# Kernel optimization log

Measured on AMD Instinct MI355X. Metric: run time of the kernel, lower is better.

The kernel has to match this reference:

```python
import jax, jax.numpy as jnp
import numpy as np

B, N, C, G, K = 4, 6000, 91, 32, 100
IMG = 800.0
SCORE_TH = 0.05
NMS_TH = 0.5
MATCH_TH = 0.5
MIN_SIZE = 0.01
BBOX_CLIP = float(np.log(1000.0 / 16.0))
WX, WY, WW, WH = 10.0, 10.0, 5.0, 5.0


def _make_boxes(key, shape_prefix):
    k1, k2 = jax.random.split(key)
    xy = jax.random.uniform(k1, shape_prefix + (2,), minval=0.0, maxval=IMG - 130.0)
    wh = jax.random.uniform(k2, shape_prefix + (2,), minval=8.0, maxval=128.0)
    return jnp.concatenate([xy, xy + wh], axis=-1)


def setup_inputs() -> dict:
    key = jax.random.key(0)
    k1, k2, k3, k4, k5 = jax.random.split(key, 5)
    return {
        "class_logits": 2.0 * jax.random.normal(k1, (B * N, C), dtype=jnp.float32),
        "box_regression": jax.random.normal(k2, (B * N, C * 4), dtype=jnp.float32),
        "proposals": _make_boxes(k3, (B, N)),
        "gt_boxes": _make_boxes(k4, (B, G)),
        "gt_labels": jax.random.randint(k5, (B, G), 1, C),
    }


def _box_iou(a, b):
    # a [G,4], b [N,4] -> [G,N]
    area_a = (a[:, 2] - a[:, 0]) * (a[:, 3] - a[:, 1])
    area_b = (b[:, 2] - b[:, 0]) * (b[:, 3] - b[:, 1])
    lt = jnp.maximum(a[:, None, :2], b[None, :, :2])
    rb = jnp.minimum(a[:, None, 2:], b[None, :, 2:])
    wh = jnp.clip(rb - lt, 0.0)
    inter = wh[..., 0] * wh[..., 1]
    return inter / (area_a[:, None] + area_b[None, :] - inter)


def _decode(rel, props):
    # torchvision BoxCoder.decode; rel [N,C,4], props [N,4]
    w = props[:, 2] - props[:, 0]
    h = props[:, 3] - props[:, 1]
    cx = props[:, 0] + 0.5 * w
    cy = props[:, 1] + 0.5 * h
    dx = rel[..., 0] / WX
    dy = rel[..., 1] / WY
    dw = jnp.minimum(rel[..., 2] / WW, BBOX_CLIP)
    dh = jnp.minimum(rel[..., 3] / WH, BBOX_CLIP)
    pcx = dx * w[:, None] + cx[:, None]
    pcy = dy * h[:, None] + cy[:, None]
    pw = jnp.exp(dw) * w[:, None]
    ph = jnp.exp(dh) * h[:, None]
    return jnp.stack([pcx - 0.5 * pw, pcy - 0.5 * ph, pcx + 0.5 * pw, pcy + 0.5 * ph], axis=-1)


def _image(logits, reg, props, gtb, gtl):
    # --- assign_targets_to_proposals (Matcher, low=high=0.5, no low-quality matches) ---
    iou = _box_iou(gtb, props)                      # [G, N]
    best = iou.max(axis=0)
    mi = jnp.argmax(iou, axis=0)
    matched = jnp.where(best >= MATCH_TH, mi, -1)   # -1 == BELOW_LOW_THRESHOLD
    assigned = jnp.where(matched >= 0, gtl[jnp.clip(matched, 0)], 0)

    # --- postprocess_detections ---
    scores = jax.nn.softmax(logits, axis=-1)[:, 1:].reshape(-1)                       # [N*(C-1)]
    boxes = jnp.clip(_decode(reg.reshape(N, C, 4), props)[:, 1:], 0.0, IMG)
    boxes = boxes.reshape(-1, 4)                                                      # [N*(C-1),4]
    labels = jnp.tile(jnp.arange(1, C), N)                                            # [N*(C-1)]
    ws = boxes[:, 2] - boxes[:, 0]
    hs = boxes[:, 3] - boxes[:, 1]
    valid = (scores > SCORE_TH) & (ws >= MIN_SIZE) & (hs >= MIN_SIZE)
    s0 = jnp.where(valid, scores, -jnp.inf)
    # batched_nms trick: offset boxes by label so cross-class IoU is 0
    off = boxes + (labels.astype(boxes.dtype) * (IMG + 1.0))[:, None]
    off_area = (off[:, 2] - off[:, 0]) * (off[:, 3] - off[:, 1])

    def step(s, _):
        i = jnp.argmax(s)
        sc = s[i]
        b = off[i]
        lt = jnp.maximum(off[:, :2], b[:2])
        rb = jnp.minimum(off[:, 2:], b[2:])
        wh = jnp.clip(rb - lt, 0.0)
        inter = wh[:, 0] * wh[:, 1]
        iou_all = inter / (off_area + (b[2] - b[0]) * (b[3] - b[1]) - inter)
        s = jnp.where(iou_all > NMS_TH, -jnp.inf, s)  # suppress (includes self)
        ok = jnp.isfinite(sc)
        ob = jnp.where(ok, boxes[i], 0.0)
        osc = jnp.where(ok, sc, 0.0)
        ol = jnp.where(ok, labels[i], -1)
        return s, (ob, osc, ol)

    _, (kb, ksc, kl) = jax.lax.scan(step, s0, None, length=K)
    return kb, ksc, kl, assigned, matched


def reference(class_logits, box_regression, proposals, gt_boxes, gt_labels):
    logits = class_logits.reshape(B, N, C)
    reg = box_regression.reshape(B, N, C * 4)
    kb, ksc, kl, assigned, matched = jax.vmap(_image)(logits, reg, proposals, gt_boxes, gt_labels)
    dets = jnp.concatenate([kb, ksc[..., None]], axis=-1)  # [B, K, 5]
    return dets, kl, assigned, matched
```

## Files before the change

### kernel.cpp

```cpp
#include <hip/hip_runtime.h>
#include <math.h>

#define NB 4
#define NN 6000
#define NC 91
#define NG 32
#define NK 100
#define NCLS (NC - 1)
#define NBUC (NB * NCLS)
#define NWRD 94
#define NWRD_P 96
#define PMAX 512
#define MATW 256
#define MPB 4096
#define RS_BLOCKS 6000

#define SCORE_TH 0.05f
#define NMS_TH 0.5f
#define MATCH_TH 0.5f
#define MIN_SIZE 0.01f
#define BBOX_CLIP 4.135166556742356f
#define C_SUP 0.5000000298023223876953125

#define CFENCE() asm volatile("" ::: "memory")

__device__ __forceinline__ bool decode_one(
    const float* __restrict__ reg, const float* __restrict__ props,
    float l, float m, float s0, int row, int c, float out[5])
{
    float score = __fdiv_rn(expf(__fsub_rn(l, m)), s0);

    const float4 p = *reinterpret_cast<const float4*>(props + (size_t)row * 4);
    float w  = __fsub_rn(p.z, p.x);
    float h  = __fsub_rn(p.w, p.y);
    float cx = __fadd_rn(p.x, __fmul_rn(0.5f, w));
    float cy = __fadd_rn(p.y, __fmul_rn(0.5f, h));

    const float4 r4 = *reinterpret_cast<const float4*>(
        reg + (size_t)row * (NC * 4) + (size_t)c * 4);
    float dx = __fdiv_rn(r4.x, 10.0f);
    float dy = __fdiv_rn(r4.y, 10.0f);
    float dw = fminf(__fdiv_rn(r4.z, 5.0f), BBOX_CLIP);
    float dh = fminf(__fdiv_rn(r4.w, 5.0f), BBOX_CLIP);

    float pcx = __fadd_rn(__fmul_rn(dx, w), cx);
    float pcy = __fadd_rn(__fmul_rn(dy, h), cy);
    float pw  = __fmul_rn(expf(dw), w);
    float ph  = __fmul_rn(expf(dh), h);

    float x1 = __fsub_rn(pcx, __fmul_rn(0.5f, pw));
    float y1 = __fsub_rn(pcy, __fmul_rn(0.5f, ph));
    float x2 = __fadd_rn(pcx, __fmul_rn(0.5f, pw));
    float y2 = __fadd_rn(pcy, __fmul_rn(0.5f, ph));
    x1 = fminf(fmaxf(x1, 0.0f), 800.0f);
    y1 = fminf(fmaxf(y1, 0.0f), 800.0f);
    x2 = fminf(fmaxf(x2, 0.0f), 800.0f);
    y2 = fminf(fmaxf(y2, 0.0f), 800.0f);

    out[0] = score; out[1] = x1; out[2] = y1; out[3] = x2; out[4] = y2;
    float ws_ = __fsub_rn(x2, x1);
    float hs_ = __fsub_rn(y2, y1);
    return (score > SCORE_TH) && (ws_ >= MIN_SIZE) && (hs_ >= MIN_SIZE);
}

__global__ __launch_bounds__(256) void fused_kernel(
    const float* __restrict__ logits, const float* __restrict__ reg,
    const float* __restrict__ props, const float* __restrict__ gtb,
    const int* __restrict__ gtl,
    float* __restrict__ out_assigned, float* __restrict__ out_matched,
    unsigned long long* __restrict__ masks, float* __restrict__ ent)
{
    int bid = blockIdx.x;
    if (bid < RS_BLOCKS) {
        int wid = threadIdx.x >> 6, lane = threadIdx.x & 63;
        int row = bid * 4 + wid;
        const float* rp = logits + (size_t)row * NC;
        float l0 = rp[lane];
        float l1 = (lane < NC - 64) ? rp[64 + lane] : -INFINITY;
        float m = fmaxf(fmaxf(-INFINITY, l0), l1);
        for (int o = 32; o; o >>= 1) m = fmaxf(m, __shfl_down(m, o));
        m = __shfl(m, 0);
        float s = __fadd_rn(__fadd_rn(0.0f, expf(__fsub_rn(l0, m))),
                            expf(__fsub_rn(l1, m)));
        for (int o = 32; o; o >>= 1) s = __fadd_rn(s, __shfl_down(s, o));
        float s0 = __shfl(s, 0);
        float thr = __fadd_rn(m, logf(__fmul_rn(0.04f, s0)));

        int b = row / NN;
        int nprop = row - b * NN;

        if (lane >= 1 && l0 > thr) {
            float o[5];
            if (decode_one(reg, props, l0, m, s0, row, lane, o)) {
                int g = b * NCLS + (lane - 1);
                float* e = ent + ((size_t)g * NN + nprop) * 8;
                *reinterpret_cast<float4*>(e) =
                    make_float4(o[1], o[2], o[3], o[4]);
                *reinterpret_cast<float2*>(e + 4) =
                    make_float2(o[0], (float)(nprop * NCLS + (lane - 1)));
                atomicOr(&masks[(size_t)g * NWRD_P + (nprop >> 6)],
                         1ull << (nprop & 63));
            }
        }
        if (lane < NC - 64 && l1 > thr) {
            float o[5];
            int c = lane + 64;
            if (decode_one(reg, props, l1, m, s0, row, c, o)) {
                int g = b * NCLS + (c - 1);
                float* e = ent + ((size_t)g * NN + nprop) * 8;
                *reinterpret_cast<float4*>(e) =
                    make_float4(o[1], o[2], o[3], o[4]);
                *reinterpret_cast<float2*>(e + 4) =
                    make_float2(o[0], (float)(nprop * NCLS + (c - 1)));
                atomicOr(&masks[(size_t)g * NWRD_P + (nprop >> 6)],
                         1ull << (nprop & 63));
            }
        }
    } else {
        int t = (bid - RS_BLOCKS) * 256 + threadIdx.x;
        if (t >= NB * NN) return;
        int b = t / NN;
        const float4 p = *reinterpret_cast<const float4*>(props + (size_t)t * 4);
        float parea = __fmul_rn(__fsub_rn(p.z, p.x), __fsub_rn(p.w, p.y));
        float best = -1.0f; int bi = -1;
        for (int g = 0; g < NG; ++g) {
            const float4 q = *reinterpret_cast<const float4*>(gtb + ((size_t)b * NG + g) * 4);
            float garea = __fmul_rn(__fsub_rn(q.z, q.x), __fsub_rn(q.w, q.y));
            float ltx = fmaxf(q.x, p.x), lty = fmaxf(q.y, p.y);
            float rbx = fminf(q.z, p.z), rby = fminf(q.w, p.w);
            float wx = fmaxf(__fsub_rn(rbx, ltx), 0.0f);
            float wy = fmaxf(__fsub_rn(rby, lty), 0.0f);
            float inter = __fmul_rn(wx, wy);
            float iou = __fdiv_rn(inter, __fsub_rn(__fadd_rn(garea, parea), inter));
            if (iou > best) { best = iou; bi = g; }
        }
        int matched = (best >= MATCH_TH) ? bi : -1;
        int assigned = (matched >= 0) ? gtl[b * NG + matched] : 0;
        out_matched[t]  = (float)matched;
        out_assigned[t] = (float)assigned;
    }
}

__device__ void nms_glb_sparse(int g, const unsigned long long* __restrict__ M,
                               float* __restrict__ E, float tb, float cls,
                               float* __restrict__ selbuf, int* __restrict__ selcnt)
{
    int lane = threadIdx.x & 63;
    int kout = 0;
    for (int k = 0; k < NK; ++k) {
        float bv = -INFINITY, boi = INFINITY; int bi = -1;
        for (int i = lane; i < NN; i += 64) {
            if (!((M[i >> 6] >> (i & 63)) & 1ull)) continue;
            float v = E[(size_t)i * 8 + 4], oi = E[(size_t)i * 8 + 5];
            if (v > bv || (v == bv && oi < boi)) { bv = v; boi = oi; bi = i; }
        }
        int wl = lane;
        for (int o = 1; o < 64; o <<= 1) {
            float v2 = __shfl_xor(bv, o); float o2 = __shfl_xor(boi, o);
            int l2 = __shfl_xor(wl, o);
            bool bt = (v2 > bv) || (v2 == bv && o2 < boi);
            bv = bt ? v2 : bv; boi = bt ? o2 : boi; wl = bt ? l2 : wl;
        }
        if (bv == -INFINITY) break;
        int wi = __shfl(bi, wl);
        float sx1 = E[(size_t)wi * 8 + 0], sy1 = E[(size_t)wi * 8 + 1];
        float sx2 = E[(size_t)wi * 8 + 2], sy2 = E[(size_t)wi * 8 + 3];
        if (lane == wl) {
            float* so = selbuf + ((size_t)g * NK + k) * 8;
            so[0] = bv; so[1] = sx1; so[2] = sy1; so[3] = sx2; so[4] = sy2;
            so[5] = cls; so[6] = boi; so[7] = 0.0f;
        }
        float bx1 = __fadd_rn(sx1, tb), by1 = __fadd_rn(sy1, tb);
        float bx2 = __fadd_rn(sx2, tb), by2 = __fadd_rn(sy2, tb);
        float sar = __fmul_rn(__fsub_rn(bx2, bx1), __fsub_rn(by2, by1));
        for (int i = lane; i < NN; i += 64) {
            if (!((M[i >> 6] >> (i & 63)) & 1ull)) continue;
            float v = E[(size_t)i * 8 + 4];
            if (v == -INFINITY) continue;
            float ox1 = __fadd_rn(E[(size_t)i * 8 + 0], tb);
            float oy1 = __fadd_rn(E[(size_t)i * 8 + 1], tb);
            float ox2 = __fadd_rn(E[(size_t)i * 8 + 2], tb);
            float oy2 = __fadd_rn(E[(size_t)i * 8 + 3], tb);
            float oar = __fmul_rn(__fsub_rn(ox2, ox1), __fsub_rn(oy2, oy1));
            float ltx = fmaxf(ox1, bx1), lty = fmaxf(oy1, by1);
            float rbx = fminf(ox2, bx2), rby = fminf(oy2, by2);
            float wx = fmaxf(__fsub_rn(rbx, ltx), 0.0f);
            float wy = fmaxf(__fsub_rn(rby, lty), 0.0f);
            float inter = __fmul_rn(wx, wy);
            float den = __fsub_rn(__fadd_rn(oar, sar), inter);
            if ((double)inter > C_SUP * (double)den) E[(size_t)i * 8 + 4] = -INFINITY;
        }
        kout = k + 1;
    }
    if (lane == 0) selcnt[g] = kout;
}

template <int CAP>
__device__ __forceinline__ float selN(const float a[CAP], int j) {
    float r = a[0];
#pragma unroll
    for (int i = 1; i < CAP; ++i) r = (j == i) ? a[i] : r;
    return r;
}
__device__ __forceinline__ float rdlane(float v, int l) {
    return __uint_as_float(
        (unsigned)__builtin_amdgcn_readlane((int)__float_as_uint(v), l));
}
__device__ __forceinline__ unsigned long long rdlane64(unsigned long long v, int l) {
    unsigned lo = (unsigned)__builtin_amdgcn_readlane((int)(unsigned)v, l);
    unsigned hi = (unsigned)__builtin_amdgcn_readlane((int)(unsigned)(v >> 32), l);
    return ((unsigned long long)hi << 32) | lo;
}

template <int CAP>
__device__ __forceinline__ int sweep_reg(
    int lane, int n, float tb,
    const float* sx1, const float* sy1, const float* sx2, const float* sy2,
    int* acc)
{
    float ox1[CAP], oy1[CAP], ox2[CAP], oy2[CAP], oar[CAP];
    unsigned alive = 0;
#pragma unroll
    for (int j = 0; j < CAP; ++j) {
        int sidx = lane * CAP + j;
        if (sidx < n) {
            float a  = __fadd_rn(sx1[sidx], tb);
            float b_ = __fadd_rn(sy1[sidx], tb);
            float c_ = __fadd_rn(sx2[sidx], tb);
            float d_ = __fadd_rn(sy2[sidx], tb);
            ox1[j] = a; oy1[j] = b_; ox2[j] = c_; oy2[j] = d_;
            oar[j] = __fmul_rn(__fsub_rn(c_, a), __fsub_rn(d_, b_));
            alive |= 1u << j;
        } else {
            ox1[j] = 0.f; oy1[j] = 0.f; ox2[j] = 0.f; oy2[j] = 0.f; oar[j] = 0.f;
        }
    }
    int kout = 0;
    while (kout < NK) {
        unsigned long long bal = __ballot(alive != 0u);
        if (!bal) break;
        int fl = (int)__ffsll(bal) - 1;
        unsigned am = (unsigned)__builtin_amdgcn_readlane((int)alive, fl);
        int js = __ffs(am) - 1;
        float bx1 = rdlane(selN<CAP>(ox1, js), fl);
        float by1 = rdlane(selN<CAP>(oy1, js), fl);
        float bx2 = rdlane(selN<CAP>(ox2, js), fl);
        float by2 = rdlane(selN<CAP>(oy2, js), fl);
        float bar = rdlane(selN<CAP>(oar, js), fl);
        if (lane == 0) acc[kout] = fl * CAP + js;
        kout++;
        unsigned kill = 0;
#pragma unroll
        for (int j = 0; j < CAP; ++j) {
            float ltx = fmaxf(ox1[j], bx1), lty = fmaxf(oy1[j], by1);
            float rbx = fminf(ox2[j], bx2), rby = fminf(oy2[j], by2);
            float wx = fmaxf(__fsub_rn(rbx, ltx), 0.0f);
            float wy = fmaxf(__fsub_rn(rby, lty), 0.0f);
            float inter = __fmul_rn(wx, wy);
            float den = __fsub_rn(__fadd_rn(oar[j], bar), inter);
            if ((double)inter > C_SUP * (double)den) kill |= 1u << j;
        }
        alive &= ~kill;
    }
    return kout;
}

__global__ __launch_bounds__(512) void bucket_nms_kernel(
    const unsigned long long* __restrict__ masks,
    float* __restrict__ entries,
    float* __restrict__ selbuf, int* __restrict__ selcnt)
{
    int g = blockIdx.x;
    int tid = threadIdx.x;
    float* E = entries + (size_t)g * NN * 8;
    const unsigned long long* M = masks + (size_t)g * NWRD_P;
    float cls = (float)(g % NCLS + 1);
    float tb = __fmul_rn(cls, 801.0f);

    __shared__ int sidx[PMAX];
    __shared__ int woff[NWRD + 1];
    __shared__ unsigned skhi[PMAX], sklo[PMAX];
    __shared__ int sperm[PMAX];
    __shared__ float sx1[PMAX], sy1[PMAX], sx2[PMAX], sy2[PMAX];
    __shared__ unsigned long long dmask[MATW * 4];
    __shared__ int acc[NK];
    __shared__ int s_kout, s_fb;

    unsigned long long myw = (tid < NWRD) ? M[tid] : 0ull;
    if (tid < NWRD) woff[tid] = __popcll(myw);
    __syncthreads();
    if (tid == 0) {
        int a = 0;
        for (int w = 0; w < NWRD; ++w) { int c = woff[w]; woff[w] = a; a += c; }
        woff[NWRD] = a;
    }
    __syncthreads();
    int n = woff[NWRD];
    if (n == 0) { if (tid == 0) selcnt[g] = 0; return; }
    if (n > PMAX) {
        if (tid < 64) nms_glb_sparse(g, M, E, tb, cls, selbuf, selcnt);
        return;
    }
    if (tid < NWRD) {
        unsigned long long m = myw;
        int base = woff[tid], r = 0;
        while (m) {
            int b = (int)__ffsll(m) - 1;
            sidx[base + r] = tid * 64 + b;
            r++; m &= m - 1;
        }
    }
    __syncthreads();

    int P = 64; while (P < n) P <<= 1;

    for (int i = tid; i < P; i += 512) {
        if (i < n) {
            const float2 kv = *reinterpret_cast<const float2*>(
                E + (size_t)sidx[i] * 8 + 4);
            skhi[i] = __float_as_uint(kv.x);
            sklo[i] = ~((unsigned)kv.y);
        } else { skhi[i] = 0u; sklo[i] = 0u; }
        sperm[i] = i;
    }
    __syncthreads();
    for (int k = 2; k <= P; k <<= 1) {
        for (int j = k >> 1; j > 0; j >>= 1) {
            bool cross = (j >= 128);
            if (cross) __syncthreads();
            for (int t = tid; t < (P >> 1); t += 512) {
                int i = ((t & ~(j - 1)) << 1) | (t & (j - 1));
                int l = i | j;
                unsigned ah = skhi[i], al = sklo[i], ch = skhi[l], cl_ = sklo[l];
                bool alt = (ah < ch) || (ah == ch && al < cl_);
                bool agt = (ah > ch) || (ah == ch && al > cl_);
                bool sw = ((i & k) == 0) ? alt : agt;
                if (sw) {
                    skhi[i] = ch; sklo[i] = cl_; skhi[l] = ah; sklo[l] = al;
                    int tp = sperm[i]; sperm[i] = sperm[l]; sperm[l] = tp;
                }
            }
            if (cross) __syncthreads();
            else CFENCE();
        }
    }
    __syncthreads();
    for (int i = tid; i < n; i += 512) {
        const float4 v = *reinterpret_cast<const float4*>(
            E + (size_t)sidx[sperm[i]] * 8);
        sx1[i] = v.x; sy1[i] = v.y; sx2[i] = v.z; sy2[i] = v.w;
    }
    __syncthreads();

    int W = (n < MATW) ? n : MATW;
    int nchunk = (W + 63) >> 6;
    int wv = tid >> 6, lane = tid & 63;

    float jx1[4], jy1[4], jx2[4], jy2[4], jar[4];
#pragma unroll
    for (int c = 0; c < 4; ++c) {
        int j = c * 64 + lane;
        if (j < W) {
            float a  = __fadd_rn(sx1[j], tb);
            float b_ = __fadd_rn(sy1[j], tb);
            float c_ = __fadd_rn(sx2[j], tb);
            float d_ = __fadd_rn(sy2[j], tb);
            jx1[c] = a; jy1[c] = b_; jx2[c] = c_; jy2[c] = d_;
            jar[c] = __fmul_rn(__fsub_rn(c_, a), __fsub_rn(d_, b_));
        } else {
            jx1[c] = 0.f; jy1[c] = 0.f; jx2[c] = 0.f; jy2[c] = 0.f; jar[c] = 0.f;
        }
    }
    {
        int i0 = wv;
        float nx1 = 0.f, ny1 = 0.f, nx2 = 0.f, ny2 = 0.f;
        if (i0 < W) { nx1 = sx1[i0]; ny1 = sy1[i0]; nx2 = sx2[i0]; ny2 = sy2[i0]; }
        for (int i = i0; i < W; i += 8) {
            float rx1 = nx1, ry1 = ny1, rx2 = nx2, ry2 = ny2;
            int ni = i + 8;
            if (ni < W) { nx1 = sx1[ni]; ny1 = sy1[ni]; nx2 = sx2[ni]; ny2 = sy2[ni]; }
            float bx1 = __fadd_rn(rx1, tb), by1 = __fadd_rn(ry1, tb);
            float bx2 = __fadd_rn(rx2, tb), by2 = __fadd_rn(ry2, tb);
            float bar = __fmul_rn(__fsub_rn(bx2, bx1), __fsub_rn(by2, by1));
            int ic = i >> 6;
#pragma unroll
            for (int c = 0; c < 4; ++c) {
                if (c >= ic && c < nchunk) {
                    bool jv = (c * 64 + lane) < W;
                    float ltx = fmaxf(jx1[c], bx1), lty = fmaxf(jy1[c], by1);
                    float rbx = fminf(jx2[c], bx2), rby = fminf(jy2[c], by2);
                    float wx = fmaxf(__fsub_rn(rbx, ltx), 0.0f);
                    float wy = fmaxf(__fsub_rn(rby, lty), 0.0f);
                    float inter = __fmul_rn(wx, wy);
                    float den = __fsub_rn(__fadd_rn(jar[c], bar), inter);
                    bool sup = jv && ((double)inter > C_SUP * (double)den);
                    unsigned long long w64 = __ballot(sup);
                    if (lane == 0) dmask[i * 4 + c] = w64;
                }
            }
        }
    }
    __syncthreads();

    if (tid < 64) {
        unsigned long long a0 = 0, a1 = 0, a2 = 0, a3 = 0;
        {
            int rem = W;
            a0 = (rem >= 64) ? ~0ull : ((rem > 0) ? ((1ull << rem) - 1) : 0); rem -= 64;
            a1 = (rem >= 64) ? ~0ull : ((rem > 0) ? ((1ull << rem) - 1) : 0); rem -= 64;
            a2 = (rem >= 64) ? ~0ull : ((rem > 0) ? ((1ull << rem) - 1) : 0); rem -= 64;
            a3 = (rem >= 64) ? ~0ull : ((rem > 0) ? ((1ull << rem) - 1) : 0);
        }
        int kout = 0;
        while (kout < NK) {
            int cand;
            if      (a0) cand = (int)__ffsll(a0) - 1;
            else if (a1) cand = 64  + (int)__ffsll(a1) - 1;
            else if (a2) cand = 128 + (int)__ffsll(a2) - 1;
            else if (a3) cand = 192 + (int)__ffsll(a3) - 1;
            else break;
            if (lane == 0) acc[kout] = cand;
            kout++;
            unsigned long long mrow = (lane < 4) ? dmask[cand * 4 + lane] : 0ull;
            a0 &= ~rdlane64(mrow, 0);
            a1 &= ~rdlane64(mrow, 1);
            a2 &= ~rdlane64(mrow, 2);
            a3 &= ~rdlane64(mrow, 3);
        }
        if (lane == 0) {
            s_kout = kout;
            s_fb = (kout < NK && n > W) ? 1 : 0;
        }
    }
    __syncthreads();

    if (s_fb) {
        if (tid < 64) {
            int kout = sweep_reg<8>(lane, n, tb, sx1, sy1, sx2, sy2, acc);
            if (lane == 0) s_kout = kout;
        }
        __syncthreads();
    }

    int kc = s_kout;
    if (tid == 0) selcnt[g] = kc;
    for (int k = tid; k < kc; k += 512) {
        int cand = acc[k];
        float* so = selbuf + ((size_t)g * NK + k) * 8;
        so[0] = __uint_as_float(skhi[cand]);
        so[1] = sx1[cand]; so[2] = sy1[cand];
        so[3] = sx2[cand]; so[4] = sy2[cand];
        so[5] = cls; so[6] = (float)(~sklo[cand]); so[7] = 0.0f;
    }
}

__global__ __launch_bounds__(512) void merge_kernel(
    const float* __restrict__ selbuf, const int* __restrict__ selcnt,
    float* __restrict__ out_dets, float* __restrict__ out_kl)
{
    int b = blockIdx.x, tid = threadIdx.x;
    __shared__ int scnt[NCLS], soff[NCLS + 1];
    __shared__ unsigned akhi[512], aklo[512];
    __shared__ unsigned bkhi[MPB], bklo[MPB], bpay[MPB];
    __shared__ int s_T, s_cntA;
    __shared__ unsigned s_LBhi, s_LBlo;

    if (tid < NCLS) scnt[tid] = selcnt[b * NCLS + tid];
    if (tid == 0) s_T = 0;
    __syncthreads();
    if (tid == 0) {
        int a = 0, ca = 0;
        for (int c = 0; c < NCLS; ++c) {
            soff[c] = a; a += scnt[c];
            ca += (scnt[c] < 4 ? scnt[c] : 4);
        }
        soff[NCLS] = a; s_cntA = ca;
    }
    __syncthreads();
    int tot = soff[NCLS];

    if (tot == 0) {
        for (int z = tid; z < NK * 5; z += 512) out_dets[(size_t)b * NK * 5 + z] = 0.0f;
        for (int z = tid; z < NK; z += 512)     out_kl[(size_t)b * NK + z] = -1.0f;
        return;
    }

    {
        unsigned kh = 0u, kl = 0u;
        if (tid < NCLS * 4) {
            int c = tid >> 2, i = tid & 3;
            if (i < scnt[c]) {
                const float* e = selbuf + ((size_t)(b * NCLS + c) * NK + i) * 8;
                kh = __float_as_uint(e[0]); kl = ~((unsigned)e[6]);
            }
        }
        akhi[tid] = kh; aklo[tid] = kl;
    }
    __syncthreads();
    for (int k = 2; k <= 512; k <<= 1) {
        for (int j = k >> 1; j > 0; j >>= 1) {
            bool cross = (j >= 128);
            if (cross) __syncthreads();
            if (tid < 256) {
                int t = tid;
                int i = ((t & ~(j - 1)) << 1) | (t & (j - 1));
                int l = i | j;
                unsigned ah = akhi[i], al = aklo[i], ch = akhi[l], cl_ = aklo[l];
                bool alt = (ah < ch) || (ah == ch && al < cl_);
                bool agt = (ah > ch) || (ah == ch && al > cl_);
                bool sw = ((i & k) == 0) ? alt : agt;
                if (sw) {
                    akhi[i] = ch; aklo[i] = cl_; akhi[l] = ah; aklo[l] = al;
                }
            }
            if (cross) __syncthreads();
            else CFENCE();
        }
    }
    __syncthreads();
    if (tid == 0) {
        if (s_cntA >= NK) { s_LBhi = akhi[NK - 1]; s_LBlo = aklo[NK - 1]; }
        else              { s_LBhi = 0u;           s_LBlo = 0u; }
    }
    __syncthreads();
    unsigned LBhi = s_LBhi, LBlo = s_LBlo;

    for (int flat = tid; flat < tot; flat += 512) {
        int lo = 0, hi = NCLS - 1;
        while (lo < hi) { int mid = (lo + hi + 1) >> 1;
                          if (soff[mid] <= flat) lo = mid; else hi = mid - 1; }
        int c = lo, i = flat - soff[c];
        const float* e = selbuf + ((size_t)(b * NCLS + c) * NK + i) * 8;
        unsigned kh = __float_as_uint(e[0]), kl = ~((unsigned)e[6]);
        bool ge = (kh > LBhi) || (kh == LBhi && kl >= LBlo);
        if (ge) {
            int pos = atomicAdd(&s_T, 1);
            if (pos < MPB) { bkhi[pos] = kh; bklo[pos] = kl;
                             bpay[pos] = (unsigned)((c << 7) | i); }
        }
    }
    __syncthreads();
    int T = s_T;

    if (T > MPB) {
        if (tid >= 64) return;
        int lane = tid;
        int g0 = b * NCLS + lane;
        int g1 = (lane < NCLS - 64) ? g0 + 64 : -1;
        int c0 = scnt[lane];
        int c1 = (g1 >= 0) ? scnt[lane + 64] : 0;
        int p0 = 0, p1 = 0;
        unsigned long long k0c = 0, k1c = 0;
        if (p0 < c0) { const float* h = selbuf + ((size_t)g0 * NK) * 8;
            k0c = ((unsigned long long)__float_as_uint(h[0]) << 32) | (unsigned long long)(~(unsigned)h[6]); }
        if (g1 >= 0 && p1 < c1) { const float* h = selbuf + ((size_t)g1 * NK) * 8;
            k1c = ((unsigned long long)__float_as_uint(h[0]) << 32) | (unsigned long long)(~(unsigned)h[6]); }
        for (int k = 0; k < NK; ++k) {
            bool t1 = (k1c > k0c);
            unsigned long long bk = t1 ? k1c : k0c;
            int bslot = t1 ? (lane + 64) : lane;
            for (int o = 1; o < 64; o <<= 1) {
                unsigned long long k2 = __shfl_xor(bk, o);
                int b2 = __shfl_xor(bslot, o);
                if (k2 > bk) { bk = k2; bslot = b2; }
            }
            if (bk == 0ull) {
                for (int z = k * 5 + lane; z < NK * 5; z += 64)
                    out_dets[(size_t)b * NK * 5 + z] = 0.0f;
                for (int z = k + lane; z < NK; z += 64)
                    out_kl[(size_t)b * NK + z] = -1.0f;
                return;
            }
            int owner = bslot & 63;
            if (lane == owner) {
                bool isA = (bslot < 64);
                int gg = isA ? g0 : g1;
                int pp = isA ? p0 : p1;
                const float* e = selbuf + ((size_t)gg * NK + pp) * 8;
                size_t o = ((size_t)b * NK + k) * 5;
                out_dets[o + 0] = e[1]; out_dets[o + 1] = e[2];
                out_dets[o + 2] = e[3]; out_dets[o + 3] = e[4];
                out_dets[o + 4] = e[0];
                out_kl[(size_t)b * NK + k] = e[5];
                if (isA) {
                    p0++; k0c = 0;
                    if (p0 < c0) { const float* h = selbuf + ((size_t)g0 * NK + p0) * 8;
                        k0c = ((unsigned long long)__float_as_uint(h[0]) << 32) | (unsigned long long)(~(unsigned)h[6]); }
                } else {
                    p1++; k1c = 0;
                    if (p1 < c1) { const float* h = selbuf + ((size_t)g1 * NK + p1) * 8;
                        k1c = ((unsigned long long)__float_as_uint(h[0]) << 32) | (unsigned long long)(~(unsigned)h[6]); }
                }
            }
        }
        return;
    }

    int P = 128; while (P < T) P <<= 1;
    for (int i = T + tid; i < P; i += 512) { bkhi[i] = 0u; bklo[i] = 0u; bpay[i] = 0u; }
    __syncthreads();
    for (int k = 2; k <= P; k <<= 1) {
        for (int j = k >> 1; j > 0; j >>= 1) {
            bool cross = (j >= 128);
            if (cross) __syncthreads();
            for (int t = tid; t < (P >> 1); t += 512) {
                int i = ((t & ~(j - 1)) << 1) | (t & (j - 1));
                int l = i | j;
                unsigned ah = bkhi[i], al = bklo[i], ch = bkhi[l], cl_ = bklo[l];
                bool alt = (ah < ch) || (ah == ch && al < cl_);
                bool agt = (ah > ch) || (ah == ch && al > cl_);
                bool sw = ((i & k) == 0) ? alt : agt;
                if (sw) {
                    bkhi[i] = ch; bklo[i] = cl_; bkhi[l] = ah; bklo[l] = al;
                    unsigned tp = bpay[i]; bpay[i] = bpay[l]; bpay[l] = tp;
                }
            }
            if (cross) __syncthreads();
            else CFENCE();
        }
    }
    __syncthreads();
    int kc = (T < NK) ? T : NK;
    for (int k = tid; k < NK; k += 512) {
        size_t o = ((size_t)b * NK + k) * 5;
        if (k < kc) {
            unsigned pay = bpay[k];
            int c = (int)(pay >> 7), p = (int)(pay & 127);
            const float* e = selbuf + ((size_t)(b * NCLS + c) * NK + p) * 8;
            out_dets[o + 0] = e[1]; out_dets[o + 1] = e[2];
            out_dets[o + 2] = e[3]; out_dets[o + 3] = e[4];
            out_dets[o + 4] = e[0];
            out_kl[(size_t)b * NK + k] = e[5];
        } else {
            out_dets[o + 0] = 0.0f; out_dets[o + 1] = 0.0f;
            out_dets[o + 2] = 0.0f; out_dets[o + 3] = 0.0f;
            out_dets[o + 4] = 0.0f;
            out_kl[(size_t)b * NK + k] = -1.0f;
        }
    }
}

extern "C" void kernel_launch(void* const* d_in, const int* in_sizes, int n_in,
                              void* d_out, int out_size, void* d_ws, size_t ws_size,
                              hipStream_t stream) {
    const float* logits = (const float*)d_in[0];
    const float* reg    = (const float*)d_in[1];
    const float* props  = (const float*)d_in[2];
    const float* gtb    = (const float*)d_in[3];
    const int*   gtl    = (const int*)d_in[4];

    float* out          = (float*)d_out;
    float* out_dets     = out;
    float* out_kl       = out + NB * NK * 5;
    float* out_assigned = out_kl + NB * NK;
    float* out_matched  = out_assigned + NB * NN;

    char* ws = (char*)d_ws;
    int*   selcnt  = (int*)(ws + 0);
    float* selbuf  = (float*)(ws + 65536);
    unsigned long long* masks =
        (unsigned long long*)(ws + 2097152);
    float* entries = (float*)(ws + 8388608);

    hipMemsetAsync(masks, 0, (size_t)NBUC * NWRD_P * sizeof(unsigned long long),
                   stream);
    const int MATCH_BLOCKS = (NB * NN + 255) / 256;
    fused_kernel<<<RS_BLOCKS + MATCH_BLOCKS, 256, 0, stream>>>(
        logits, reg, props, gtb, gtl, out_assigned, out_matched,
        masks, entries);
    bucket_nms_kernel<<<NBUC, 512, 0, stream>>>(
        masks, entries, selbuf, selcnt);
    merge_kernel<<<NB, 512, 0, stream>>>(selbuf, selcnt, out_dets, out_kl);
}
```

Before: 115.4 us.

## Fuse per-image merge into bucket NMS via last-block-done atomic counter

Removes the separate merge kernel launch. Each bucket NMS block increments a per-image completion counter after a threadfence, and the last block to finish for an image performs the merge using shared memory unioned with the bucket scratch. The counter is zeroed by extending the existing memset. This saves one launch and its gap, but the merge for each image now runs serialized at the tail of one block, and the shared-memory union may change occupancy.

Result: slower. 163.1 us (median of 3 runs) (+41.4%).

```diff
diff --git a/kernel.cpp b/kernel.cpp
--- a/kernel.cpp
+++ b/kernel.cpp
@@ -265,219 +265,45 @@
     return kout;
 }
 
-__global__ __launch_bounds__(512) void bucket_nms_kernel(
-    const unsigned long long* __restrict__ masks,
-    float* __restrict__ entries,
-    float* __restrict__ selbuf, int* __restrict__ selcnt)
+struct BucketSmem {
+    int sidx[PMAX];
+    int woff[NWRD + 1];
+    unsigned skhi[PMAX], sklo[PMAX];
+    int sperm[PMAX];
+    float sx1[PMAX], sy1[PMAX], sx2[PMAX], sy2[PMAX];
+    unsigned long long dmask[MATW * 4];
+    int acc[NK];
+    int s_kout, s_fb;
+};
+struct MergeSmem {
+    int scnt[NCLS], soff[NCLS + 1];
+    unsigned akhi[512], aklo[512];
+    unsigned bkhi[MPB], bklo[MPB], bpay[MPB];
+    int s_T, s_cntA;
+    unsigned s_LBhi, s_LBlo;
+};
+union SmemU { BucketSmem bk; MergeSmem mg; };
+
+__device__ void merge_image(int b, MergeSmem& sm,
+                            const float* __restrict__ selbuf,
+                            const int* __restrict__ selcnt,
+                            float* __restrict__ out_dets,
+                            float* __restrict__ out_kl)
 {
-    int g = blockIdx.x;
     int tid = threadIdx.x;
-    float* E = entries + (size_t)g * NN * 8;
-    const unsigned long long* M = masks + (size_t)g * NWRD_P;
-    float cls = (float)(g % NCLS + 1);
-    float tb = __fmul_rn(cls, 801.0f);
-
-    __shared__ int sidx[PMAX];
-    __shared__ int woff[NWRD + 1];
-    __shared__ unsigned skhi[PMAX], sklo[PMAX];
-    __shared__ int sperm[PMAX];
-    __shared__ float sx1[PMAX], sy1[PMAX], sx2[PMAX], sy2[PMAX];
-    __shared__ unsigned long long dmask[MATW * 4];
-    __shared__ int acc[NK];
-    __shared__ int s_kout, s_fb;
-
-    unsigned long long myw = (tid < NWRD) ? M[tid] : 0ull;
-    if (tid < NWRD) woff[tid] = __popcll(myw);
-    __syncthreads();
-    if (tid == 0) {
-        int a = 0;
-        for (int w = 0; w < NWRD; ++w) { int c = woff[w]; woff[w] = a; a += c; }
-        woff[NWRD] = a;
-    }
-    __syncthreads();
-    int n = woff[NWRD];
-    if (n == 0) { if (tid == 0) selcnt[g] = 0; return; }
-    if (n > PMAX) {
-        if (tid < 64) nms_glb_sparse(g, M, E, tb, cls, selbuf, selcnt);
-        return;
-    }
-    if (tid < NWRD) {
-        unsigned long long m = myw;
-        int base = woff[tid], r = 0;
-        while (m) {
-            int b = (int)__ffsll(m) - 1;
-            sidx[base + r] = tid * 64 + b;
-            r++; m &= m - 1;
-        }
-    }
-    __syncthreads();
-
-    int P = 64; while (P < n) P <<= 1;
-
-    for (int i = tid; i < P; i += 512) {
-        if (i < n) {
-            const float2 kv = *reinterpret_cast<const float2*>(
-                E + (size_t)sidx[i] * 8 + 4);
-            skhi[i] = __float_as_uint(kv.x);
-            sklo[i] = ~((unsigned)kv.y);
-        } else { skhi[i] = 0u; sklo[i] = 0u; }
-        sperm[i] = i;
-    }
-    __syncthreads();
-    for (int k = 2; k <= P; k <<= 1) {
-        for (int j = k >> 1; j > 0; j >>= 1) {
-            bool cross = (j >= 128);
-            if (cross) __syncthreads();
-            for (int t = tid; t < (P >> 1); t += 512) {
-                int i = ((t & ~(j - 1)) << 1) | (t & (j - 1));
-                int l = i | j;
-                unsigned ah = skhi[i], al = sklo[i], ch = skhi[l], cl_ = sklo[l];
-                bool alt = (ah < ch) || (ah == ch && al < cl_);
-                bool agt = (ah > ch) || (ah == ch && al > cl_);
-                bool sw = ((i & k) == 0) ? alt : agt;
-                if (sw) {
-                    skhi[i] = ch; sklo[i] = cl_; skhi[l] = ah; sklo[l] = al;
-                    int tp = sperm[i]; sperm[i] = sperm[l]; sperm[l] = tp;
-                }
-            }
-            if (cross) __syncthreads();
-            else CFENCE();
-        }
-    }
-    __syncthreads();
-    for (int i = tid; i < n; i += 512) {
-        const float4 v = *reinterpret_cast<const float4*>(
-            E + (size_t)sidx[sperm[i]] * 8);
-        sx1[i] = v.x; sy1[i] = v.y; sx2[i] = v.z; sy2[i] = v.w;
-    }
-    __syncthreads();
-
-    int W = (n < MATW) ? n : MATW;
-    int nchunk = (W + 63) >> 6;
-    int wv = tid >> 6, lane = tid & 63;
-
-    float jx1[4], jy1[4], jx2[4], jy2[4], jar[4];
-#pragma unroll
-    for (int c = 0; c < 4; ++c) {
-        int j = c * 64 + lane;
-        if (j < W) {
-            float a  = __fadd_rn(sx1[j], tb);
-            float b_ = __fadd_rn(sy1[j], tb);
-            float c_ = __fadd_rn(sx2[j], tb);
-            float d_ = __fadd_rn(sy2[j], tb);
-            jx1[c] = a; jy1[c] = b_; jx2[c] = c_; jy2[c] = d_;
-            jar[c] = __fmul_rn(__fsub_rn(c_, a), __fsub_rn(d_, b_));
-        } else {
-            jx1[c] = 0.f; jy1[c] = 0.f; jx2[c] = 0.f; jy2[c] = 0.f; jar[c] = 0.f;
-        }
-    }
-    {
-        int i0 = wv;
-        float nx1 = 0.f, ny1 = 0.f, nx2 = 0.f, ny2 = 0.f;
-        if (i0 < W) { nx1 = sx1[i0]; ny1 = sy1[i0]; nx2 = sx2[i0]; ny2 = sy2[i0]; }
-        for (int i = i0; i < W; i += 8) {
-            float rx1 = nx1, ry1 = ny1, rx2 = nx2, ry2 = ny2;
-            int ni = i + 8;
-            if (ni < W) { nx1 = sx1[ni]; ny1 = sy1[ni]; nx2 = sx2[ni]; ny2 = sy2[ni]; }
-            float bx1 = __fadd_rn(rx1, tb), by1 = __fadd_rn(ry1, tb);
-            float bx2 = __fadd_rn(rx2, tb), by2 = __fadd_rn(ry2, tb);
-            float bar = __fmul_rn(__fsub_rn(bx2, bx1), __fsub_rn(by2, by1));
-            int ic = i >> 6;
-#pragma unroll
-            for (int c = 0; c < 4; ++c) {
-                if (c >= ic && c < nchunk) {
-                    bool jv = (c * 64 + lane) < W;
-                    float ltx = fmaxf(jx1[c], bx1), lty = fmaxf(jy1[c], by1);
-                    float rbx = fminf(jx2[c], bx2), rby = fminf(jy2[c], by2);
-                    float wx = fmaxf(__fsub_rn(rbx, ltx), 0.0f);
-                    float wy = fmaxf(__fsub_rn(rby, lty), 0.0f);
-                    float inter = __fmul_rn(wx, wy);
-                    float den = __fsub_rn(__fadd_rn(jar[c], bar), inter);
-                    bool sup = jv && ((double)inter > C_SUP * (double)den);
-                    unsigned long long w64 = __ballot(sup);
-                    if (lane == 0) dmask[i * 4 + c] = w64;
-                }
-            }
-        }
-    }
-    __syncthreads();
-
-    if (tid < 64) {
-        unsigned long long a0 = 0, a1 = 0, a2 = 0, a3 = 0;
-        {
-            int rem = W;
-            a0 = (rem >= 64) ? ~0ull : ((rem > 0) ? ((1ull << rem) - 1) : 0); rem -= 64;
-            a1 = (rem >= 64) ? ~0ull : ((rem > 0) ? ((1ull << rem) - 1) : 0); rem -= 64;
-            a2 = (rem >= 64) ? ~0ull : ((rem > 0) ? ((1ull << rem) - 1) : 0); rem -= 64;
-            a3 = (rem >= 64) ? ~0ull : ((rem > 0) ? ((1ull << rem) - 1) : 0);
-        }
-        int kout = 0;
-        while (kout < NK) {
-            int cand;
-            if      (a0) cand = (int)__ffsll(a0) - 1;
-            else if (a1) cand = 64  + (int)__ffsll(a1) - 1;
-            else if (a2) cand = 128 + (int)__ffsll(a2) - 1;
-            else if (a3) cand = 192 + (int)__ffsll(a3) - 1;
-            else break;
-            if (lane == 0) acc[kout] = cand;
-            kout++;
-            unsigned long long mrow = (lane < 4) ? dmask[cand * 4 + lane] : 0ull;
-            a0 &= ~rdlane64(mrow, 0);
-            a1 &= ~rdlane64(mrow, 1);
-            a2 &= ~rdlane64(mrow, 2);
-            a3 &= ~rdlane64(mrow, 3);
-        }
-        if (lane == 0) {
-            s_kout = kout;
-            s_fb = (kout < NK && n > W) ? 1 : 0;
-        }
-    }
-    __syncthreads();
-
-    if (s_fb) {
-        if (tid < 64) {
-            int kout = sweep_reg<8>(lane, n, tb, sx1, sy1, sx2, sy2, acc);
-            if (lane == 0) s_kout = kout;
-        }
-        __syncthreads();
-    }
-
-    int kc = s_kout;
-    if (tid == 0) selcnt[g] = kc;
-    for (int k = tid; k < kc; k += 512) {
-        int cand = acc[k];
-        float* so = selbuf + ((size_t)g * NK + k) * 8;
-        so[0] = __uint_as_float(skhi[cand]);
-        so[1] = sx1[cand]; so[2] = sy1[cand];
-        so[3] = sx2[cand]; so[4] = sy2[cand];
-        so[5] = cls; so[6] = (float)(~sklo[cand]); so[7] = 0.0f;
-    }
-}
-
-__global__ __launch_bounds__(512) void merge_kernel(
-    const float* __restrict__ selbuf, const int* __restrict__ selcnt,
-    float* __restrict__ out_dets, float* __restrict__ out_kl)
-{
-    int b = blockIdx.x, tid = threadIdx.x;
-    __shared__ int scnt[NCLS], soff[NCLS + 1];
-    __shared__ unsigned akhi[512], aklo[512];
-    __shared__ unsigned bkhi[MPB], bklo[MPB], bpay[MPB];
-    __shared__ int s_T, s_cntA;
-    __shared__ unsigned s_LBhi, s_LBlo;
-
-    if (tid < NCLS) scnt[tid] = selcnt[b * NCLS + tid];
-    if (tid == 0) s_T = 0;
+    if (tid < NCLS) sm.scnt[tid] = selcnt[b * NCLS + tid];
+    if (tid == 0) sm.s_T = 0;
     __syncthreads();
     if (tid == 0) {
         int a = 0, ca = 0;
         for (int c = 0; c < NCLS; ++c) {
-            soff[c] = a; a += scnt[c];
-            ca += (scnt[c] < 4 ? scnt[c] : 4);
-        }
-        soff[NCLS] = a; s_cntA = ca;
-    }
-    __syncthreads();
-    int tot = soff[NCLS];
+            sm.soff[c] = a; a += sm.scnt[c];
+            ca += (sm.scnt[c] < 4 ? sm.scnt[c] : 4);
+        }
+        sm.soff[NCLS] = a; sm.s_cntA = ca;
+    }
+    __syncthreads();
+    int tot = sm.soff[NCLS];
 
     if (tot == 0) {
         for (int z = tid; z < NK * 5; z += 512) out_dets[(size_t)b * NK * 5 + z] = 0.0f;
@@ -489,12 +315,12 @@
         unsigned kh = 0u, kl = 0u;
         if (tid < NCLS * 4) {
             int c = tid >> 2, i = tid & 3;
-            if (i < scnt[c]) {
+            if (i < sm.scnt[c]) {
                 const float* e = selbuf + ((size_t)(b * NCLS + c) * NK + i) * 8;
                 kh = __float_as_uint(e[0]); kl = ~((unsigned)e[6]);
             }
         }
-        akhi[tid] = kh; aklo[tid] = kl;
+        sm.akhi[tid] = kh; sm.aklo[tid] = kl;
     }
     __syncthreads();
     for (int k = 2; k <= 512; k <<= 1) {
@@ -505,12 +331,14 @@
                 int t = tid;
                 int i = ((t & ~(j - 1)) << 1) | (t & (j - 1));
                 int l = i | j;
-                unsigned ah = akhi[i], al = aklo[i], ch = akhi[l], cl_ = aklo[l];
+                unsigned ah = sm.akhi[i], al = sm.aklo[i];
+                unsigned ch = sm.akhi[l], cl_ = sm.aklo[l];
                 bool alt = (ah < ch) || (ah == ch && al < cl_);
                 bool agt = (ah > ch) || (ah == ch && al > cl_);
                 bool sw = ((i & k) == 0) ? alt : agt;
                 if (sw) {
-                    akhi[i] = ch; aklo[i] = cl_; akhi[l] = ah; aklo[l] = al;
+                    sm.akhi[i] = ch; sm.aklo[i] = cl_;
+                    sm.akhi[l] = ah; sm.aklo[l] = al;
                 }
             }
             if (cross) __syncthreads();
@@ -519,36 +347,36 @@
     }
     __syncthreads();
     if (tid == 0) {
-        if (s_cntA >= NK) { s_LBhi = akhi[NK - 1]; s_LBlo = aklo[NK - 1]; }
-        else              { s_LBhi = 0u;           s_LBlo = 0u; }
-    }
-    __syncthreads();
-    unsigned LBhi = s_LBhi, LBlo = s_LBlo;
+        if (sm.s_cntA >= NK) { sm.s_LBhi = sm.akhi[NK - 1]; sm.s_LBlo = sm.aklo[NK - 1]; }
+        else                 { sm.s_LBhi = 0u;              sm.s_LBlo = 0u; }
+    }
+    __syncthreads();
+    unsigned LBhi = sm.s_LBhi, LBlo = sm.s_LBlo;
 
     for (int flat = tid; flat < tot; flat += 512) {
         int lo = 0, hi = NCLS - 1;
         while (lo < hi) { int mid = (lo + hi + 1) >> 1;
-                          if (soff[mid] <= flat) lo = mid; else hi = mid - 1; }
-        int c = lo, i = flat - soff[c];
+                          if (sm.soff[mid] <= flat) lo = mid; else hi = mid - 1; }
+        int c = lo, i = flat - sm.soff[c];
         const float* e = selbuf + ((size_t)(b * NCLS + c) * NK + i) * 8;
         unsigned kh = __float_as_uint(e[0]), kl = ~((unsigned)e[6]);
         bool ge = (kh > LBhi) || (kh == LBhi && kl >= LBlo);
         if (ge) {
-            int pos = atomicAdd(&s_T, 1);
-            if (pos < MPB) { bkhi[pos] = kh; bklo[pos] = kl;
-                             bpay[pos] = (unsigned)((c << 7) | i); }
-        }
-    }
-    __syncthreads();
-    int T = s_T;
+            int pos = atomicAdd(&sm.s_T, 1);
+            if (pos < MPB) { sm.bkhi[pos] = kh; sm.bklo[pos] = kl;
+                             sm.bpay[pos] = (unsigned)((c << 7) | i); }
+        }
+    }
+    __syncthreads();
+    int T = sm.s_T;
 
     if (T > MPB) {
         if (tid >= 64) return;
         int lane = tid;
         int g0 = b * NCLS + lane;
         int g1 = (lane < NCLS - 64) ? g0 + 64 : -1;
-        int c0 = scnt[lane];
-        int c1 = (g1 >= 0) ? scnt[lane + 64] : 0;
+        int c0 = sm.scnt[lane];
+        int c1 = (g1 >= 0) ? sm.scnt[lane + 64] : 0;
         int p0 = 0, p1 = 0;
         unsigned long long k0c = 0, k1c = 0;
         if (p0 < c0) { const float* h = selbuf + ((size_t)g0 * NK) * 8;
@@ -597,7 +425,7 @@
     }
 
     int P = 128; while (P < T) P <<= 1;
-    for (int i = T + tid; i < P; i += 512) { bkhi[i] = 0u; bklo[i] = 0u; bpay[i] = 0u; }
+    for (int i = T + tid; i < P; i += 512) { sm.bkhi[i] = 0u; sm.bklo[i] = 0u; sm.bpay[i] = 0u; }
     __syncthreads();
     for (int k = 2; k <= P; k <<= 1) {
         for (int j = k >> 1; j > 0; j >>= 1) {
@@ -606,13 +434,15 @@
             for (int t = tid; t < (P >> 1); t += 512) {
                 int i = ((t & ~(j - 1)) << 1) | (t & (j - 1));
                 int l = i | j;
-                unsigned ah = bkhi[i], al = bklo[i], ch = bkhi[l], cl_ = bklo[l];
+                unsigned ah = sm.bkhi[i], al = sm.bklo[i];
+                unsigned ch = sm.bkhi[l], cl_ = sm.bklo[l];
                 bool alt = (ah < ch) || (ah == ch && al < cl_);
                 bool agt = (ah > ch) || (ah == ch && al > cl_);
                 bool sw = ((i & k) == 0) ? alt : agt;
                 if (sw) {
-                    bkhi[i] = ch; bklo[i] = cl_; bkhi[l] = ah; bklo[l] = al;
-                    unsigned tp = bpay[i]; bpay[i] = bpay[l]; bpay[l] = tp;
+                    sm.bkhi[i] = ch; sm.bklo[i] = cl_;
+                    sm.bkhi[l] = ah; sm.bklo[l] = al;
+                    unsigned tp = sm.bpay[i]; sm.bpay[i] = sm.bpay[l]; sm.bpay[l] = tp;
                 }
             }
             if (cross) __syncthreads();
@@ -624,7 +454,7 @@
     for (int k = tid; k < NK; k += 512) {
         size_t o = ((size_t)b * NK + k) * 5;
         if (k < kc) {
-            unsigned pay = bpay[k];
+            unsigned pay = sm.bpay[k];
             int c = (int)(pay >> 7), p = (int)(pay & 127);
             const float* e = selbuf + ((size_t)(b * NCLS + c) * NK + p) * 8;
             out_dets[o + 0] = e[1]; out_dets[o + 1] = e[2];
@@ -640,6 +470,211 @@
     }
 }
 
+__global__ __launch_bounds__(512) void bucket_nms_kernel(
+    const unsigned long long* __restrict__ masks,
+    float* __restrict__ entries,
+    float* __restrict__ selbuf, int* __restrict__ selcnt,
+    int* __restrict__ done,
+    float* __restrict__ out_dets, float* __restrict__ out_kl)
+{
+    int g = blockIdx.x;
+    int tid = threadIdx.x;
+    int bimg = g / NCLS;
+    float* E = entries + (size_t)g * NN * 8;
+    const unsigned long long* M = masks + (size_t)g * NWRD_P;
+    float cls = (float)(g % NCLS + 1);
+    float tb = __fmul_rn(cls, 801.0f);
+
+    __shared__ SmemU sm;
+    __shared__ int s_win;
+
+    unsigned long long myw = (tid < NWRD) ? M[tid] : 0ull;
+    if (tid < NWRD) sm.bk.woff[tid] = __popcll(myw);
+    __syncthreads();
+    if (tid == 0) {
+        int a = 0;
+        for (int w = 0; w < NWRD; ++w) { int c = sm.bk.woff[w]; sm.bk.woff[w] = a; a += c; }
+        sm.bk.woff[NWRD] = a;
+    }
+    __syncthreads();
+    int n = sm.bk.woff[NWRD];
+
+    if (n == 0) {
+        if (tid == 0) selcnt[g] = 0;
+    } else if (n > PMAX) {
+        if (tid < 64) nms_glb_sparse(g, M, E, tb, cls, selbuf, selcnt);
+    } else {
+        if (tid < NWRD) {
+            unsigned long long m = myw;
+            int base = sm.bk.woff[tid], r = 0;
+            while (m) {
+                int b = (int)__ffsll(m) - 1;
+                sm.bk.sidx[base + r] = tid * 64 + b;
+                r++; m &= m - 1;
+            }
+        }
+        __syncthreads();
+
+        int P = 64; while (P < n) P <<= 1;
+
+        for (int i = tid; i < P; i += 512) {
+            if (i < n) {
+                const float2 kv = *reinterpret_cast<const float2*>(
+                    E + (size_t)sm.bk.sidx[i] * 8 + 4);
+                sm.bk.skhi[i] = __float_as_uint(kv.x);
+                sm.bk.sklo[i] = ~((unsigned)kv.y);
+            } else { sm.bk.skhi[i] = 0u; sm.bk.sklo[i] = 0u; }
+            sm.bk.sperm[i] = i;
+        }
+        __syncthreads();
+        for (int k = 2; k <= P; k <<= 1) {
+            for (int j = k >> 1; j > 0; j >>= 1) {
+                bool cross = (j >= 128);
+                if (cross) __syncthreads();
+                for (int t = tid; t < (P >> 1); t += 512) {
+                    int i = ((t & ~(j - 1)) << 1) | (t & (j - 1));
+                    int l = i | j;
+                    unsigned ah = sm.bk.skhi[i], al = sm.bk.sklo[i];
+                    unsigned ch = sm.bk.skhi[l], cl_ = sm.bk.sklo[l];
+                    bool alt = (ah < ch) || (ah == ch && al < cl_);
+                    bool agt = (ah > ch) || (ah == ch && al > cl_);
+                    bool sw = ((i & k) == 0) ? alt : agt;
+                    if (sw) {
+                        sm.bk.skhi[i] = ch; sm.bk.sklo[i] = cl_;
+                        sm.bk.skhi[l] = ah; sm.bk.sklo[l] = al;
+                        int tp = sm.bk.sperm[i]; sm.bk.sperm[i] = sm.bk.sperm[l];
+                        sm.bk.sperm[l] = tp;
+                    }
+                }
+                if (cross) __syncthreads();
+                else CFENCE();
+            }
+        }
+        __syncthreads();
+        for (int i = tid; i < n; i += 512) {
+            const float4 v = *reinterpret_cast<const float4*>(
+                E + (size_t)sm.bk.sidx[sm.bk.sperm[i]] * 8);
+            sm.bk.sx1[i] = v.x; sm.bk.sy1[i] = v.y;
+            sm.bk.sx2[i] = v.z; sm.bk.sy2[i] = v.w;
+        }
+        __syncthreads();
+
+        int W = (n < MATW) ? n : MATW;
+        int nchunk = (W + 63) >> 6;
+        int wv = tid >> 6, lane = tid & 63;
+
+        float jx1[4], jy1[4], jx2[4], jy2[4], jar[4];
+#pragma unroll
+        for (int c = 0; c < 4; ++c) {
+            int j = c * 64 + lane;
+            if (j < W) {
+                float a  = __fadd_rn(sm.bk.sx1[j], tb);
+                float b_ = __fadd_rn(sm.bk.sy1[j], tb);
+                float c_ = __fadd_rn(sm.bk.sx2[j], tb);
+                float d_ = __fadd_rn(sm.bk.sy2[j], tb);
+                jx1[c] = a; jy1[c] = b_; jx2[c] = c_; jy2[c] = d_;
+                jar[c] = __fmul_rn(__fsub_rn(c_, a), __fsub_rn(d_, b_));
+            } else {
+                jx1[c] = 0.f; jy1[c] = 0.f; jx2[c] = 0.f; jy2[c] = 0.f; jar[c] = 0.f;
+            }
+        }
+        {
+            int i0 = wv;
+            float nx1 = 0.f, ny1 = 0.f, nx2 = 0.f, ny2 = 0.f;
+            if (i0 < W) { nx1 = sm.bk.sx1[i0]; ny1 = sm.bk.sy1[i0];
+                          nx2 = sm.bk.sx2[i0]; ny2 = sm.bk.sy2[i0]; }
+            for (int i = i0; i < W; i += 8) {
+                float rx1 = nx1, ry1 = ny1, rx2 = nx2, ry2 = ny2;
+                int ni = i + 8;
+                if (ni < W) { nx1 = sm.bk.sx1[ni]; ny1 = sm.bk.sy1[ni];
+                              nx2 = sm.bk.sx2[ni]; ny2 = sm.bk.sy2[ni]; }
+                float bx1 = __fadd_rn(rx1, tb), by1 = __fadd_rn(ry1, tb);
+                float bx2 = __fadd_rn(rx2, tb), by2 = __fadd_rn(ry2, tb);
+                float bar = __fmul_rn(__fsub_rn(bx2, bx1), __fsub_rn(by2, by1));
+                int ic = i >> 6;
+#pragma unroll
+                for (int c = 0; c < 4; ++c) {
+                    if (c >= ic && c < nchunk) {
+                        bool jv = (c * 64 + lane) < W;
+                        float ltx = fmaxf(jx1[c], bx1), lty = fmaxf(jy1[c], by1);
+                        float rbx = fminf(jx2[c], bx2), rby = fminf(jy2[c], by2);
+                        float wx = fmaxf(__fsub_rn(rbx, ltx), 0.0f);
+                        float wy = fmaxf(__fsub_rn(rby, lty), 0.0f);
+                        float inter = __fmul_rn(wx, wy);
+                        float den = __fsub_rn(__fadd_rn(jar[c], bar), inter);
+                        bool sup = jv && ((double)inter > C_SUP * (double)den);
+                        unsigned long long w64 = __ballot(sup);
+                        if (lane == 0) sm.bk.dmask[i * 4 + c] = w64;
+                    }
+                }
+            }
+        }
+        __syncthreads();
+
+        if (tid < 64) {
+            unsigned long long a0 = 0, a1 = 0, a2 = 0, a3 = 0;
+            {
+                int rem = W;
+                a0 = (rem >= 64) ? ~0ull : ((rem > 0) ? ((1ull << rem) - 1) : 0); rem -= 64;
+                a1 = (rem >= 64) ? ~0ull : ((rem > 0) ? ((1ull << rem) - 1) : 0); rem -= 64;
+                a2 = (rem >= 64) ? ~0ull : ((rem > 0) ? ((1ull << rem) - 1) : 0); rem -= 64;
+                a3 = (rem >= 64) ? ~0ull : ((rem > 0) ? ((1ull << rem) - 1) : 0);
+            }
+            int kout = 0;
+            while (kout < NK) {
+                int cand;
+                if      (a0) cand = (int)__ffsll(a0) - 1;
+                else if (a1) cand = 64  + (int)__ffsll(a1) - 1;
+                else if (a2) cand = 128 + (int)__ffsll(a2) - 1;
+                else if (a3) cand = 192 + (int)__ffsll(a3) - 1;
+                else break;
+                if (lane == 0) sm.bk.acc[kout] = cand;
+                kout++;
+                unsigned long long mrow = (lane < 4) ? sm.bk.dmask[cand * 4 + lane] : 0ull;
+                a0 &= ~rdlane64(mrow, 0);
+                a1 &= ~rdlane64(mrow, 1);
+                a2 &= ~rdlane64(mrow, 2);
+                a3 &= ~rdlane64(mrow, 3);
+            }
+            if (lane == 0) {
+                sm.bk.s_kout = kout;
+                sm.bk.s_fb = (kout < NK && n > W) ? 1 : 0;
+            }
+        }
+        __syncthreads();
+
+        if (sm.bk.s_fb) {
+            if (tid < 64) {
+                int kout = sweep_reg<8>(tid & 63, n, tb, sm.bk.sx1, sm.bk.sy1,
+                                        sm.bk.sx2, sm.bk.sy2, sm.bk.acc);
+                if ((tid & 63) == 0) sm.bk.s_kout = kout;
+            }
+            __syncthreads();
+        }
+
+        int kc = sm.bk.s_kout;
+        if (tid == 0) selcnt[g] = kc;
+        for (int k = tid; k < kc; k += 512) {
+            int cand = sm.bk.acc[k];
+            float* so = selbuf + ((size_t)g * NK + k) * 8;
+            so[0] = __uint_as_float(sm.bk.skhi[cand]);
+            so[1] = sm.bk.sx1[cand]; so[2] = sm.bk.sy1[cand];
+            so[3] = sm.bk.sx2[cand]; so[4] = sm.bk.sy2[cand];
+            so[5] = cls; so[6] = (float)(~sm.bk.sklo[cand]); so[7] = 0.0f;
+        }
+    }
+
+    __syncthreads();
+    __threadfence();
+    if (tid == 0)
+        s_win = (atomicAdd(&done[bimg], 1) == NCLS - 1) ? 1 : 0;
+    __syncthreads();
+    if (s_win) {
+        __threadfence();
+        merge_image(bimg, sm.mg, selbuf, selcnt, out_dets, out_kl);
+    }
+}
+
 extern "C" void kernel_launch(void* const* d_in, const int* in_sizes, int n_in,
                               void* d_out, int out_size, void* d_ws, size_t ws_size,
                               hipStream_t stream) {
@@ -658,17 +693,18 @@
     char* ws = (char*)d_ws;
     int*   selcnt  = (int*)(ws + 0);
     float* selbuf  = (float*)(ws + 65536);
+    int*   done    = (int*)(ws + 2093056);
     unsigned long long* masks =
         (unsigned long long*)(ws + 2097152);
     float* entries = (float*)(ws + 8388608);
 
-    hipMemsetAsync(masks, 0, (size_t)NBUC * NWRD_P * sizeof(unsigned long long),
+    hipMemsetAsync(ws + 2093056, 0,
+                   4096 + (size_t)NBUC * NWRD_P * sizeof(unsigned long long),
                    stream);
     const int MATCH_BLOCKS = (NB * NN + 255) / 256;
     fused_kernel<<<RS_BLOCKS + MATCH_BLOCKS, 256, 0, stream>>>(
         logits, reg, props, gtb, gtl, out_assigned, out_matched,
         masks, entries);
     bucket_nms_kernel<<<NBUC, 512, 0, stream>>>(
-        masks, entries, selbuf, selcnt);
-    merge_kernel<<<NB, 512, 0, stream>>>(selbuf, selcnt, out_dets, out_kl);
-}
+        masks, entries, selbuf, selcnt, done, out_dets, out_kl);
+}
```
